# Kernel tuning notes

Hardware: AMD Instinct MI355X
Metric: run time of the kernel (lower is better)

The kernel has to match this reference:

```python
import jax, jax.numpy as jnp
import numpy as np


def setup_inputs() -> dict:
    key = jax.random.key(0)
    k1, k2 = jax.random.split(key)
    N, M, D = 8192, 8192, 3
    set1 = jax.random.normal(k1, (N, D), dtype=jnp.float32)
    set2 = jax.random.normal(k2, (M, D), dtype=jnp.float32)
    return {
        "set1": set1,
        "set2": set2,
        "hausdorff": 0,      # 0 -> averaged Hausdorff, 1 -> proper Hausdorff
        "w_set1_set2": 1,    # nonzero -> compute set1->set2 direction
        "w_set2_set1": 1,    # nonzero -> compute set2->set1 direction
        "n_outputs": 1,      # 1 -> return sum, 2 -> return tuple
    }


def _directional_terms(set1, set2, hausdorff, w12, w21):
    # Pairwise Euclidean distances: [N, M]
    diff = set1[:, None, :] - set2[None, :, :]          # [N, M, d]
    d2 = jnp.sqrt(jnp.sum(diff * diff, axis=-1))        # [N, M]
    reduce = jnp.mean if hausdorff == 0 else jnp.max
    zero = jnp.zeros([], dtype=d2.dtype)
    t12 = reduce(jnp.min(d2, axis=1)) if w12 != 0 else zero
    t21 = reduce(jnp.min(d2, axis=0)) if w21 != 0 else zero
    return t12, t21


def reference(set1, set2, hausdorff, w_set1_set2, w_set2_set1, n_outputs):
    t12, t21 = _directional_terms(set1, set2, hausdorff, w_set1_set2, w_set2_set1)
    if n_outputs == 1:
        return t12 + t21
    return (t12, t21)
```

## Files before the change

kernel.cpp:

```cpp
#include <hip/hip_runtime.h>
#include <math.h>

#define BLK    256
#define SRCB   32
#define SPT    8
#define TILE   512

__global__ void __launch_bounds__(BLK, 2)
hd_min_kernel(const float* __restrict__ s1, int n1,
              const float* __restrict__ s2, int n2,
              float2* __restrict__ bpart, int nbx) {
    const int dir = blockIdx.y;
    const float* src = dir ? s2 : s1;
    const float* tgt = dir ? s1 : s2;
    const int nSrc   = dir ? n2 : n1;
    const int nTgt   = dir ? n1 : n2;

    const int w    = threadIdx.x >> 6;
    const int lane = threadIdx.x & 63;
    const int base = blockIdx.x * SRCB + w * SPT;

    float sx[SPT], sy[SPT], sz[SPT], sw[SPT];
    #pragma unroll
    for (int k = 0; k < SPT; ++k) {
        const int i = base + k;
        float x = 0.f, y = 0.f, z = 0.f;
        if (i < nSrc) { x = src[3*i]; y = src[3*i+1]; z = src[3*i+2]; }
        sx[k] = -x; sy[k] = -y; sz[k] = -z;
        sw[k] = 0.5f * fmaf(z, z, fmaf(y, y, x * x));
    }

    float m[SPT];
    #pragma unroll
    for (int k = 0; k < SPT; ++k) m[k] = INFINITY;

    __shared__ float4 ldsT[TILE];

    for (int tile = 0; tile < nTgt; tile += TILE) {
        #pragma unroll
        for (int r = 0; r < TILE / BLK; ++r) {
            const int idx = r * BLK + threadIdx.x;
            const int j = tile + idx;
            float x = 0.f, y = 0.f, z = 0.f, tw;
            if (j < nTgt) {
                x = tgt[3*j]; y = tgt[3*j+1]; z = tgt[3*j+2];
                tw = 0.5f * fmaf(z, z, fmaf(y, y, x * x));
            } else {
                tw = INFINITY;
            }
            ldsT[idx] = make_float4(x, y, z, tw);
        }
        __syncthreads();

        #pragma unroll
        for (int c = 0; c < TILE / 64; ++c) {
            const float4 t = ldsT[c * 64 + lane];
            #pragma unroll
            for (int k = 0; k < SPT; ++k) {
                const float v = fmaf(t.x, sx[k], fmaf(t.y, sy[k], fmaf(t.z, sz[k], t.w)));
                m[k] = fminf(m[k], v);
            }
        }
        __syncthreads();
    }

    #pragma unroll
    for (int off = 1; off < 64; off <<= 1) {
        #pragma unroll
        for (int k = 0; k < SPT; ++k)
            m[k] = fminf(m[k], __shfl_xor(m[k], off));
    }

    __shared__ float ssum[BLK / 64], smax[BLK / 64];
    if (lane == 0) {
        float sum = 0.f, mx = 0.f;
        #pragma unroll
        for (int k = 0; k < SPT; ++k) {
            if (base + k < nSrc) {
                const float d = sqrtf(fmaxf(2.0f * (m[k] + sw[k]), 0.0f));
                sum += d;
                mx = fmaxf(mx, d);
            }
        }
        ssum[w] = sum; smax[w] = mx;
    }
    __syncthreads();
    if (threadIdx.x == 0) {
        float s = 0.f, mm = 0.f;
        #pragma unroll
        for (int q = 0; q < BLK / 64; ++q) { s += ssum[q]; mm = fmaxf(mm, smax[q]); }
        bpart[dir * nbx + blockIdx.x] = make_float2(s, mm);
    }
}

__global__ void hd_final_kernel(const float2* __restrict__ bpart, int nbx,
                                int n1, int n2,
                                const int* __restrict__ haus,
                                const int* __restrict__ w12,
                                const int* __restrict__ w21,
                                const int* __restrict__ nout,
                                float* __restrict__ out) {
    float s0 = 0.f, x0 = 0.f, s1 = 0.f, x1 = 0.f;
    for (int t = threadIdx.x; t < nbx; t += BLK) {
        const float2 a = bpart[t];
        const float2 b = bpart[nbx + t];
        s0 += a.x; x0 = fmaxf(x0, a.y);
        s1 += b.x; x1 = fmaxf(x1, b.y);
    }
    for (int o = 32; o > 0; o >>= 1) {
        s0 += __shfl_down(s0, o); x0 = fmaxf(x0, __shfl_down(x0, o));
        s1 += __shfl_down(s1, o); x1 = fmaxf(x1, __shfl_down(x1, o));
    }
    __shared__ float a0[BLK/64], b0[BLK/64], a1[BLK/64], b1[BLK/64];
    const int w = threadIdx.x >> 6, lane = threadIdx.x & 63;
    if (lane == 0) { a0[w] = s0; b0[w] = x0; a1[w] = s1; b1[w] = x1; }
    __syncthreads();
    if (threadIdx.x == 0) {
        float S0 = 0.f, X0 = 0.f, S1 = 0.f, X1 = 0.f;
        for (int q = 0; q < BLK/64; ++q) {
            S0 += a0[q]; X0 = fmaxf(X0, b0[q]);
            S1 += a1[q]; X1 = fmaxf(X1, b1[q]);
        }
        float t12 = 0.f, t21 = 0.f;
        if (*w12 != 0) t12 = (*haus == 0) ? S0 / (float)n1 : X0;
        if (*w21 != 0) t21 = (*haus == 0) ? S1 / (float)n2 : X1;
        if (*nout == 1) {
            out[0] = t12 + t21;
        } else {
            out[0] = t12;
            out[1] = t21;
        }
    }
}

extern "C" void kernel_launch(void* const* d_in, const int* in_sizes, int n_in,
                              void* d_out, int out_size, void* d_ws, size_t ws_size,
                              hipStream_t stream) {
    const float* s1 = (const float*)d_in[0];
    const float* s2 = (const float*)d_in[1];
    const int* haus = (const int*)d_in[2];
    const int* w12  = (const int*)d_in[3];
    const int* w21  = (const int*)d_in[4];
    const int* nout = (const int*)d_in[5];
    float* out = (float*)d_out;

    const int n1 = in_sizes[0] / 3;
    const int n2 = in_sizes[1] / 3;
    const int maxN = (n1 > n2) ? n1 : n2;
    const int nbx = (maxN + SRCB - 1) / SRCB;

    float2* bpart = (float2*)d_ws;

    dim3 grid(nbx, 2);
    hd_min_kernel<<<grid, BLK, 0, stream>>>(s1, n1, s2, n2, bpart, nbx);

    hd_final_kernel<<<1, BLK, 0, stream>>>(bpart, nbx, n1, n2,
                                           haus, w12, w21, nout, out);
}
```

Before: 26.17 us.

## Split target range across blocks and prepack points into float4

```diff
diff --git a/kernel.cpp b/kernel.cpp
--- a/kernel.cpp
+++ b/kernel.cpp
@@ -5,50 +5,63 @@
 #define SRCB   32
 #define SPT    8
 #define TILE   512
+#define NT     4
+#define NRB    32
 
-__global__ void __launch_bounds__(BLK, 2)
-hd_min_kernel(const float* __restrict__ s1, int n1,
-              const float* __restrict__ s2, int n2,
-              float2* __restrict__ bpart, int nbx) {
-    const int dir = blockIdx.y;
-    const float* src = dir ? s2 : s1;
-    const float* tgt = dir ? s1 : s2;
-    const int nSrc   = dir ? n2 : n1;
-    const int nTgt   = dir ? n1 : n2;
+__global__ void hd_pack_kernel(const float* __restrict__ s1, int n1,
+                               const float* __restrict__ s2, int n2,
+                               float4* __restrict__ p1, float4* __restrict__ p2) {
+    const int i = blockIdx.x * BLK + threadIdx.x;
+    if (i < n1) {
+        float x = s1[3 * i], y = s1[3 * i + 1], z = s1[3 * i + 2];
+        p1[i] = make_float4(x, y, z, 0.5f * fmaf(z, z, fmaf(y, y, x * x)));
+    }
+    if (i < n2) {
+        float x = s2[3 * i], y = s2[3 * i + 1], z = s2[3 * i + 2];
+        p2[i] = make_float4(x, y, z, 0.5f * fmaf(z, z, fmaf(y, y, x * x)));
+    }
+}
+
+__global__ void __launch_bounds__(BLK, 4)
+hd_min_kernel(const float4* __restrict__ p1, int n1,
+              const float4* __restrict__ p2, int n2,
+              float* __restrict__ pmin, int maxN) {
+    const int dir = blockIdx.z;
+    const float4* src = dir ? p2 : p1;
+    const float4* tgt = dir ? p1 : p2;
+    const int nSrc    = dir ? n2 : n1;
+    const int nTgt    = dir ? n1 : n2;
+
+    if (blockIdx.x * SRCB >= nSrc) return;
 
     const int w    = threadIdx.x >> 6;
     const int lane = threadIdx.x & 63;
     const int base = blockIdx.x * SRCB + w * SPT;
 
+    const int chunkLen = (nTgt + NT - 1) / NT;
+    const int cbeg = blockIdx.y * chunkLen;
+    const int cend = min(cbeg + chunkLen, nTgt);
+
     float sx[SPT], sy[SPT], sz[SPT], sw[SPT];
     #pragma unroll
     for (int k = 0; k < SPT; ++k) {
         const int i = base + k;
-        float x = 0.f, y = 0.f, z = 0.f;
-        if (i < nSrc) { x = src[3*i]; y = src[3*i+1]; z = src[3*i+2]; }
-        sx[k] = -x; sy[k] = -y; sz[k] = -z;
-        sw[k] = 0.5f * fmaf(z, z, fmaf(y, y, x * x));
+        float4 s = (i < nSrc) ? src[i] : make_float4(0.f, 0.f, 0.f, 0.f);
+        sx[k] = -s.x; sy[k] = -s.y; sz[k] = -s.z; sw[k] = s.w;
     }
-
     float m[SPT];
     #pragma unroll
     for (int k = 0; k < SPT; ++k) m[k] = INFINITY;
 
     __shared__ float4 ldsT[TILE];
 
-    for (int tile = 0; tile < nTgt; tile += TILE) {
+    for (int tile = cbeg; tile < cend; tile += TILE) {
         #pragma unroll
         for (int r = 0; r < TILE / BLK; ++r) {
             const int idx = r * BLK + threadIdx.x;
             const int j = tile + idx;
-            float x = 0.f, y = 0.f, z = 0.f, tw;
-            if (j < nTgt) {
-                x = tgt[3*j]; y = tgt[3*j+1]; z = tgt[3*j+2];
-                tw = 0.5f * fmaf(z, z, fmaf(y, y, x * x));
-            } else {
-                tw = INFINITY;
-            }
-            ldsT[idx] = make_float4(x, y, z, tw);
+            ldsT[idx] = (j < cend) ? tgt[j]
+                                   : make_float4(0.f, 0.f, 0.f, INFINITY);
         }
         __syncthreads();
 
@@ -71,59 +84,70 @@
             m[k] = fminf(m[k], __shfl_xor(m[k], off));
     }
 
-    __shared__ float ssum[BLK / 64], smax[BLK / 64];
     if (lane == 0) {
-        float sum = 0.f, mx = 0.f;
+        float* dst = pmin + ((size_t)dir * NT + blockIdx.y) * (size_t)maxN + base;
         #pragma unroll
         for (int k = 0; k < SPT; ++k) {
-            if (base + k < nSrc) {
-                const float d = sqrtf(fmaxf(2.0f * (m[k] + sw[k]), 0.0f));
-                sum += d;
-                mx = fmaxf(mx, d);
-            }
+            if (base + k < nSrc)
+                dst[k] = fmaxf(2.0f * (m[k] + sw[k]), 0.0f);
         }
-        ssum[w] = sum; smax[w] = mx;
     }
+}
+
+__global__ void hd_reduce_kernel(const float* __restrict__ pmin, int maxN,
+                                 int n1, int n2, float2* __restrict__ bpart) {
+    const int dir = blockIdx.y;
+    const int n = dir ? n2 : n1;
+    const float* pm = pmin + (size_t)dir * NT * maxN;
+
+    float sum = 0.f, mx = 0.f;
+    for (int i = blockIdx.x * BLK + threadIdx.x; i < n; i += NRB * BLK) {
+        const float v0 = pm[i];
+        const float v1 = pm[(size_t)maxN + i];
+        const float v2 = pm[2 * (size_t)maxN + i];
+        const float v3 = pm[3 * (size_t)maxN + i];
+        const float d = sqrtf(fminf(fminf(v0, v1), fminf(v2, v3)));
+        sum += d;
+        mx = fmaxf(mx, d);
+    }
+    for (int o = 32; o > 0; o >>= 1) {
+        sum += __shfl_down(sum, o);
+        mx = fmaxf(mx, __shfl_down(mx, o));
+    }
+    __shared__ float ssum[BLK / 64], smax[BLK / 64];
+    const int w = threadIdx.x >> 6, lane = threadIdx.x & 63;
+    if (lane == 0) { ssum[w] = sum; smax[w] = mx; }
     __syncthreads();
     if (threadIdx.x == 0) {
         float s = 0.f, mm = 0.f;
         #pragma unroll
         for (int q = 0; q < BLK / 64; ++q) { s += ssum[q]; mm = fmaxf(mm, smax[q]); }
-        bpart[dir * nbx + blockIdx.x] = make_float2(s, mm);
+        bpart[dir * NRB + blockIdx.x] = make_float2(s, mm);
     }
 }
 
-__global__ void hd_final_kernel(const float2* __restrict__ bpart, int nbx,
+__global__ void hd_final_kernel(const float2* __restrict__ bpart,
                                 int n1, int n2,
                                 const int* __restrict__ haus,
                                 const int* __restrict__ w12,
                                 const int* __restrict__ w21,
                                 const int* __restrict__ nout,
                                 float* __restrict__ out) {
+    const int t = threadIdx.x;
     float s0 = 0.f, x0 = 0.f, s1 = 0.f, x1 = 0.f;
-    for (int t = threadIdx.x; t < nbx; t += BLK) {
+    if (t < NRB) {
         const float2 a = bpart[t];
-        const float2 b = bpart[nbx + t];
-        s0 += a.x; x0 = fmaxf(x0, a.y);
-        s1 += b.x; x1 = fmaxf(x1, b.y);
+        const float2 b = bpart[NRB + t];
+        s0 = a.x; x0 = a.y; s1 = b.x; x1 = b.y;
     }
     for (int o = 32; o > 0; o >>= 1) {
         s0 += __shfl_down(s0, o); x0 = fmaxf(x0, __shfl_down(x0, o));
         s1 += __shfl_down(s1, o); x1 = fmaxf(x1, __shfl_down(x1, o));
     }
-    __shared__ float a0[BLK/64], b0[BLK/64], a1[BLK/64], b1[BLK/64];
-    const int w = threadIdx.x >> 6, lane = threadIdx.x & 63;
-    if (lane == 0) { a0[w] = s0; b0[w] = x0; a1[w] = s1; b1[w] = x1; }
-    __syncthreads();
-    if (threadIdx.x == 0) {
-        float S0 = 0.f, X0 = 0.f, S1 = 0.f, X1 = 0.f;
-        for (int q = 0; q < BLK/64; ++q) {
-            S0 += a0[q]; X0 = fmaxf(X0, b0[q]);
-            S1 += a1[q]; X1 = fmaxf(X1, b1[q]);
-        }
+    if (t == 0) {
         float t12 = 0.f, t21 = 0.f;
-        if (*w12 != 0) t12 = (*haus == 0) ? S0 / (float)n1 : X0;
-        if (*w21 != 0) t21 = (*haus == 0) ? S1 / (float)n2 : X1;
+        if (*w12 != 0) t12 = (*haus == 0) ? s0 / (float)n1 : x0;
+        if (*w21 != 0) t21 = (*haus == 0) ? s1 / (float)n2 : x1;
         if (*nout == 1) {
             out[0] = t12 + t21;
         } else {
@@ -149,11 +173,17 @@
     const int maxN = (n1 > n2) ? n1 : n2;
     const int nbx = (maxN + SRCB - 1) / SRCB;
 
-    float2* bpart = (float2*)d_ws;
+    float4* p1 = (float4*)d_ws;
+    float4* p2 = p1 + n1;
+    float* pmin = (float*)(p2 + n2);
+    float2* bpart = (float2*)(pmin + (size_t)2 * NT * maxN);
 
-    dim3 grid(nbx, 2);
-    hd_min_kernel<<<grid, BLK, 0, stream>>>(s1, n1, s2, n2, bpart, nbx);
+    hd_pack_kernel<<<(maxN + BLK - 1) / BLK, BLK, 0, stream>>>(s1, n1, s2, n2, p1, p2);
 
-    hd_final_kernel<<<1, BLK, 0, stream>>>(bpart, nbx, n1, n2,
-                                           haus, w12, w21, nout, out);
+    dim3 grid(nbx, NT, 2);
+    hd_min_kernel<<<grid, BLK, 0, stream>>>(p1, n1, p2, n2, pmin, maxN);
+
+    hd_reduce_kernel<<<dim3(NRB, 2), BLK, 0, stream>>>(pmin, maxN, n1, n2, bpart);
+
+    hd_final_kernel<<<1, 64, 0, stream>>>(bpart, n1, n2, haus, w12, w21, nout, out);
 }
```

Result: slower. 30.28 us (+15.7%).

## Prepack points to float4 and stream targets from global without LDS

Applied to the files above, without the earlier changes.

```diff
diff --git a/kernel.cpp b/kernel.cpp
--- a/kernel.cpp
+++ b/kernel.cpp
@@ -2,66 +2,69 @@
 #include <math.h>
 
 #define BLK    256
-#define SRCB   32
-#define SPT    8
-#define TILE   512
+#define SPT    4
+#define SRCB   16
 
-__global__ void __launch_bounds__(BLK, 2)
-hd_min_kernel(const float* __restrict__ s1, int n1,
-              const float* __restrict__ s2, int n2,
+__global__ void hd_pack_kernel(const float* __restrict__ s1, int n1, int pad1,
+                               const float* __restrict__ s2, int n2, int pad2,
+                               float4* __restrict__ p1, float4* __restrict__ p2) {
+    const int i = blockIdx.x * BLK + threadIdx.x;
+    if (i < pad1) {
+        float4 v = make_float4(0.f, 0.f, 0.f, INFINITY);
+        if (i < n1) {
+            float x = s1[3*i], y = s1[3*i+1], z = s1[3*i+2];
+            v = make_float4(x, y, z, 0.5f * fmaf(z, z, fmaf(y, y, x * x)));
+        }
+        p1[i] = v;
+    }
+    if (i < pad2) {
+        float4 v = make_float4(0.f, 0.f, 0.f, INFINITY);
+        if (i < n2) {
+            float x = s2[3*i], y = s2[3*i+1], z = s2[3*i+2];
+            v = make_float4(x, y, z, 0.5f * fmaf(z, z, fmaf(y, y, x * x)));
+        }
+        p2[i] = v;
+    }
+}
+
+__global__ void __launch_bounds__(BLK, 4)
+hd_min_kernel(const float4* __restrict__ p1, int n1, int pad1,
+              const float4* __restrict__ p2, int n2, int pad2,
               float2* __restrict__ bpart, int nbx) {
     const int dir = blockIdx.y;
-    const float* src = dir ? s2 : s1;
-    const float* tgt = dir ? s1 : s2;
-    const int nSrc   = dir ? n2 : n1;
-    const int nTgt   = dir ? n1 : n2;
+    const float4* src = dir ? p2 : p1;
+    const float4* tgt = dir ? p1 : p2;
+    const int nSrc    = dir ? n2 : n1;
+    const int padT    = dir ? pad1 : pad2;
+
+    if (blockIdx.x * SRCB >= nSrc) {
+        if (threadIdx.x == 0) bpart[dir * nbx + blockIdx.x] = make_float2(0.f, 0.f);
+        return;
+    }
 
     const int w    = threadIdx.x >> 6;
     const int lane = threadIdx.x & 63;
     const int base = blockIdx.x * SRCB + w * SPT;
 
-    float sx[SPT], sy[SPT], sz[SPT], sw[SPT];
+    float sx[SPT], sy[SPT], sz[SPT], swq[SPT], m[SPT];
     #pragma unroll
     for (int k = 0; k < SPT; ++k) {
         const int i = base + k;
-        float x = 0.f, y = 0.f, z = 0.f;
-        if (i < nSrc) { x = src[3*i]; y = src[3*i+1]; z = src[3*i+2]; }
-        sx[k] = -x; sy[k] = -y; sz[k] = -z;
-        sw[k] = 0.5f * fmaf(z, z, fmaf(y, y, x * x));
+        float4 s = (i < nSrc) ? src[i] : make_float4(0.f, 0.f, 0.f, 0.f);
+        sx[k] = -s.x; sy[k] = -s.y; sz[k] = -s.z; swq[k] = s.w;
+        m[k] = INFINITY;
     }
 
-    float m[SPT];
-    #pragma unroll
-    for (int k = 0; k < SPT; ++k) m[k] = INFINITY;
-
-    __shared__ float4 ldsT[TILE];
-
-    for (int tile = 0; tile < nTgt; tile += TILE) {
+    const int C = padT >> 6;
+    const float4* tp = tgt + lane;
+    #pragma unroll 4
+    for (int c = 0; c < C; ++c) {
+        const float4 t = tp[c * 64];
         #pragma unroll
-        for (int r = 0; r < TILE / BLK; ++r) {
-            const int idx = r * BLK + threadIdx.x;
-            const int j = tile + idx;
-            float x = 0.f, y = 0.f, z = 0.f, tw;
-            if (j < nTgt) {
-                x = tgt[3*j]; y = tgt[3*j+1]; z = tgt[3*j+2];
-                tw = 0.5f * fmaf(z, z, fmaf(y, y, x * x));
-            } else {
-                tw = INFINITY;
-            }
-            ldsT[idx] = make_float4(x, y, z, tw);
+        for (int k = 0; k < SPT; ++k) {
+            const float v = fmaf(t.x, sx[k], fmaf(t.y, sy[k], fmaf(t.z, sz[k], t.w)));
+            m[k] = fminf(m[k], v);
         }
-        __syncthreads();
-
-        #pragma unroll
-        for (int c = 0; c < TILE / 64; ++c) {
-            const float4 t = ldsT[c * 64 + lane];
-            #pragma unroll
-            for (int k = 0; k < SPT; ++k) {
-                const float v = fmaf(t.x, sx[k], fmaf(t.y, sy[k], fmaf(t.z, sz[k], t.w)));
-                m[k] = fminf(m[k], v);
-            }
-        }
-        __syncthreads();
     }
 
     #pragma unroll
@@ -77,7 +80,7 @@
         #pragma unroll
         for (int k = 0; k < SPT; ++k) {
             if (base + k < nSrc) {
-                const float d = sqrtf(fmaxf(2.0f * (m[k] + sw[k]), 0.0f));
+                const float d = sqrtf(fmaxf(2.0f * (m[k] + swq[k]), 0.0f));
                 sum += d;
                 mx = fmaxf(mx, d);
             }
@@ -146,13 +149,21 @@
 
     const int n1 = in_sizes[0] / 3;
     const int n2 = in_sizes[1] / 3;
+    const int pad1 = (n1 + 63) & ~63;
+    const int pad2 = (n2 + 63) & ~63;
     const int maxN = (n1 > n2) ? n1 : n2;
+    const int padMax = (pad1 > pad2) ? pad1 : pad2;
     const int nbx = (maxN + SRCB - 1) / SRCB;
 
-    float2* bpart = (float2*)d_ws;
+    float4* p1 = (float4*)d_ws;
+    float4* p2 = p1 + pad1;
+    float2* bpart = (float2*)(p2 + pad2);
+
+    hd_pack_kernel<<<(padMax + BLK - 1) / BLK, BLK, 0, stream>>>(s1, n1, pad1,
+                                                                 s2, n2, pad2, p1, p2);
 
     dim3 grid(nbx, 2);
-    hd_min_kernel<<<grid, BLK, 0, stream>>>(s1, n1, s2, n2, bpart, nbx);
+    hd_min_kernel<<<grid, BLK, 0, stream>>>(p1, n1, pad1, p2, n2, pad2, bpart, nbx);
 
     hd_final_kernel<<<1, BLK, 0, stream>>>(bpart, nbx, n1, n2,
                                            haus, w12, w21, nout, out);
```

After: 29.28 us. 11.9% more time.
